# Kernel optimization log

Hardware: AMD Instinct MI355X
Metric: run time of the kernel (lower is better)

Reference implementation:

```python
import jax, jax.numpy as jnp
import numpy as np

N_PTS = 2048
NUM_GABOR = 2
IMG_H = 512
IMG_W = 512
CHUNK = 32  # gaussians per scan step
ALPHA_THRESH = 1.0 / 255.0


def setup_inputs() -> dict:
    key = jax.random.key(0)
    ks = jax.random.split(key, 6)
    xyz = jax.random.uniform(ks[0], (N_PTS, 2), dtype=jnp.float32) * jnp.array([IMG_W, IMG_H], jnp.float32)
    cov2d = jax.random.uniform(ks[1], (N_PTS, 3), dtype=jnp.float32)
    features_dc = jax.random.normal(ks[2], (N_PTS, 3), dtype=jnp.float32)
    opacity = jnp.ones((N_PTS, 1), jnp.float32)
    gabor_freqs = (jax.random.uniform(ks[3], (N_PTS * NUM_GABOR, 2), dtype=jnp.float32) - 0.5) * 0.002
    gabor_weights = jax.random.uniform(ks[4], (N_PTS * NUM_GABOR, 1), dtype=jnp.float32) * -5.0
    background = jnp.ones((3,), jnp.float32)
    return dict(xyz=xyz, cov2d=cov2d, features_dc=features_dc, opacity=opacity,
                gabor_freqs=gabor_freqs, gabor_weights=gabor_weights,
                background=background, H=IMG_H, W=IMG_W)


def _render(xyz, cov2d, features_dc, opacity, gabor_freqs, gabor_weights, H, W):
    n = xyz.shape[0]
    g = gabor_freqs.shape[0] // n
    dt = xyz.dtype
    # cov elements with lower bound (SLV=False branch)
    covs = cov2d + jnp.array([0.5, 0.0, 0.5], dt)
    sxx, sxy, syy = covs[:, 0], covs[:, 1], covs[:, 2]
    det = sxx * syy - sxy * sxy
    valid = det > 1e-8
    det_s = jnp.where(valid, det, 1.0)
    conic_a = syy / det_s
    conic_b = -sxy / det_s
    conic_c = sxx / det_s
    # radius from max eigenvalue (for visibility filter / radii output)
    mid = 0.5 * (sxx + syy)
    lam = mid + jnp.sqrt(jnp.maximum(mid * mid - det, 0.1))
    radii = jnp.where(valid, jnp.ceil(3.0 * jnp.sqrt(lam)), 0.0).astype(jnp.int32)

    colors = jax.nn.sigmoid(features_dc)                      # color_norm=True
    freqs = jnp.exp(gabor_freqs).reshape(n, g, 2)             # get_gabor_freqs
    gw = jax.nn.sigmoid(gabor_weights).reshape(n, g)          # get_gabor_weights

    px = (jnp.arange(W, dtype=dt) + 0.5)[None, :]             # (1, W)
    py = (jnp.arange(H, dtype=dt) + 0.5)[:, None]             # (H, 1)

    steps = n // CHUNK
    def chunked(a):
        return a.reshape((steps, CHUNK) + a.shape[1:])

    xs = (chunked(xyz[:, 0]), chunked(xyz[:, 1]),
          chunked(conic_a), chunked(conic_b), chunked(conic_c),
          chunked(opacity[:, 0]), chunked(colors),
          chunked(freqs[:, :, 0]), chunked(freqs[:, :, 1]),
          chunked(gw), chunked(valid))

    def body(acc, args):
        x, y, ca, cb, cc, op, col, fx, fy, w, vm = args
        dx = px[None, :, :] - x[:, None, None]                 # (C,1,W)
        dy = py[None, :, :] - y[:, None, None]                 # (C,H,1)
        sigma = 0.5 * (ca[:, None, None] * dx * dx + cc[:, None, None] * dy * dy) \
                + cb[:, None, None] * (dx * dy)                # (C,H,W)
        alpha = op[:, None, None] * jnp.exp(-sigma)
        alpha = jnp.minimum(alpha, 0.999)
        alpha = jnp.where((alpha < ALPHA_THRESH) | (~vm[:, None, None]), 0.0, alpha)
        # gabor modulation: 1 + sum_k w_k * cos(fx_k*dx + fy_k*dy)
        arg = fx[:, :, None, None] * dx[:, None, :, :] + fy[:, :, None, None] * dy[:, None, :, :]
        mod = 1.0 + jnp.sum(w[:, :, None, None] * jnp.cos(arg), axis=1)  # (C,H,W)
        wgt = alpha * mod
        acc = acc + jnp.einsum('nhw,nc->hwc', wgt, col)
        return acc, None

    out, _ = jax.lax.scan(body, jnp.zeros((H, W, 3), dt), xs)
    img = jnp.clip(out, 0.0, 1.0)                              # (H,W,3)
    render = jnp.transpose(img[None], (0, 3, 1, 2))            # (1,3,H,W)
    return render, radii


def reference(xyz, cov2d, features_dc, opacity, gabor_freqs, gabor_weights, background, H, W):
    render, radii = _render(xyz, cov2d, features_dc, opacity, gabor_freqs, gabor_weights, H, W)
    visibility = radii > 0
    return render, radii, visibility
```

## Files before the change

### kernel.cpp

```cpp
#include <hip/hip_runtime.h>
#include <math.h>

#define NPTS 2048
#define NG 2
#define IMG_H 512
#define IMG_W 512
#define HW (IMG_H * IMG_W)
#define RENDER_SIZE (3 * HW)
#define S_MAX 5.5412636f

__device__ __forceinline__ float sigmoidf_(float x) {
    return 1.0f / (1.0f + expf(-x));
}

__global__ void init_kernel(const float* __restrict__ cov2d, float* __restrict__ out) {
    int i = blockIdx.x * blockDim.x + threadIdx.x;
    if (i < RENDER_SIZE) out[i] = 0.0f;
    if (i < NPTS) {
        float sxx = cov2d[i * 3 + 0] + 0.5f;
        float sxy = cov2d[i * 3 + 1];
        float syy = cov2d[i * 3 + 2] + 0.5f;
        float det = __fsub_rn(__fmul_rn(sxx, syy), __fmul_rn(sxy, sxy));
        bool valid = det > 1e-8f;
        float mid = __fmul_rn(0.5f, __fadd_rn(sxx, syy));
        float t = __fsub_rn(__fmul_rn(mid, mid), det);
        t = fmaxf(t, 0.1f);
        float lam = __fadd_rn(mid, sqrtf(t));
        float r = valid ? ceilf(__fmul_rn(3.0f, sqrtf(lam))) : 0.0f;
        out[RENDER_SIZE + i] = r;
        out[RENDER_SIZE + NPTS + i] = (r > 0.0f) ? 1.0f : 0.0f;
    }
}

__global__ __launch_bounds__(64) void splat_kernel(
    const float* __restrict__ xyz, const float* __restrict__ cov2d,
    const float* __restrict__ fdc, const float* __restrict__ opac,
    const float* __restrict__ gfreq, const float* __restrict__ gwts,
    float* __restrict__ out)
{
    int p = blockIdx.x;
    float sxx = cov2d[p * 3 + 0] + 0.5f;
    float sxy = cov2d[p * 3 + 1];
    float syy = cov2d[p * 3 + 2] + 0.5f;
    float det = sxx * syy - sxy * sxy;
    if (!(det > 1e-8f)) return;

    float inv = 1.0f / det;
    float ca = syy * inv;
    float cb = -sxy * inv;
    float cc = sxx * inv;

    float xn = xyz[p * 2 + 0];
    float yn = xyz[p * 2 + 1];
    float op = opac[p];

    float c0 = sigmoidf_(fdc[p * 3 + 0]);
    float c1 = sigmoidf_(fdc[p * 3 + 1]);
    float c2 = sigmoidf_(fdc[p * 3 + 2]);

    float fx0 = expf(gfreq[(p * NG + 0) * 2 + 0]);
    float fy0 = expf(gfreq[(p * NG + 0) * 2 + 1]);
    float fx1 = expf(gfreq[(p * NG + 1) * 2 + 0]);
    float fy1 = expf(gfreq[(p * NG + 1) * 2 + 1]);
    float w0 = sigmoidf_(gwts[p * NG + 0]);
    float w1 = sigmoidf_(gwts[p * NG + 1]);

    float dxm = sqrtf(2.0f * S_MAX * sxx) + 0.01f;
    float dym = sqrtf(2.0f * S_MAX * syy) + 0.01f;
    int x0 = max(0, (int)ceilf(xn - dxm - 0.5f));
    int x1 = min(IMG_W - 1, (int)floorf(xn + dxm - 0.5f));
    int y0 = max(0, (int)ceilf(yn - dym - 0.5f));
    int y1 = min(IMG_H - 1, (int)floorf(yn + dym - 0.5f));
    int bw = x1 - x0 + 1;
    int bh = y1 - y0 + 1;
    if (bw <= 0 || bh <= 0) return;
    int area = bw * bh;

    for (int idx = threadIdx.x; idx < area; idx += 64) {
        int ix = x0 + idx % bw;
        int iy = y0 + idx / bw;
        float dx = (ix + 0.5f) - xn;
        float dy = (iy + 0.5f) - yn;
        float sigma = 0.5f * (ca * dx * dx + cc * dy * dy) + cb * (dx * dy);
        float alpha = op * expf(-sigma);
        alpha = fminf(alpha, 0.999f);
        if (alpha < (1.0f / 255.0f)) continue;
        float mod = 1.0f + w0 * cosf(fx0 * dx + fy0 * dy)
                         + w1 * cosf(fx1 * dx + fy1 * dy);
        float wgt = alpha * mod;
        int pix = iy * IMG_W + ix;
        atomicAdd(&out[pix],          wgt * c0);
        atomicAdd(&out[HW + pix],     wgt * c1);
        atomicAdd(&out[2 * HW + pix], wgt * c2);
    }
}

__global__ void clamp_kernel(float* __restrict__ out) {
    int i = blockIdx.x * blockDim.x + threadIdx.x;
    if (i < RENDER_SIZE) {
        float v = out[i];
        out[i] = fminf(fmaxf(v, 0.0f), 1.0f);
    }
}

extern "C" void kernel_launch(void* const* d_in, const int* in_sizes, int n_in,
                              void* d_out, int out_size, void* d_ws, size_t ws_size,
                              hipStream_t stream) {
    const float* xyz   = (const float*)d_in[0];
    const float* cov2d = (const float*)d_in[1];
    const float* fdc   = (const float*)d_in[2];
    const float* opac  = (const float*)d_in[3];
    const float* gfreq = (const float*)d_in[4];
    const float* gwts  = (const float*)d_in[5];
    float* out = (float*)d_out;

    int blocks = (RENDER_SIZE + 255) / 256;
    init_kernel<<<blocks, 256, 0, stream>>>(cov2d, out);
    splat_kernel<<<NPTS, 64, 0, stream>>>(xyz, cov2d, fdc, opac, gfreq, gwts, out);
    clamp_kernel<<<blocks, 256, 0, stream>>>(out);
}
```

Baseline: 79.25 us.

## Replace atomic point splatting with per-tile gather rendering in one fused kernel

Switches from per-gaussian blocks that atomically scatter into the image to per-tile blocks (32x8 pixels) that cull gaussians in chunks into shared memory and accumulate per-pixel in registers. Radii computation, zero-init and clamping are fused into the same kernel, removing two full-image passes and two launches. The trade-off is that every tile re-reads and culls all points, and each chunk adds barrier synchronisation.

After: 82.83 us. 1.05x slower.

```diff
diff --git a/kernel.cpp b/kernel.cpp
--- a/kernel.cpp
+++ b/kernel.cpp
@@ -8,99 +8,126 @@
 #define HW (IMG_H * IMG_W)
 #define RENDER_SIZE (3 * HW)
 #define S_MAX 5.5412636f
+#define ALPHA_THRESH (1.0f / 255.0f)
+
+#define TW 32
+#define TH 8
+#define TILES_X (IMG_W / TW)
+#define TILES_Y (IMG_H / TH)
+#define NTILES (TILES_X * TILES_Y)
+#define CHUNK_PTS 256
 
 __device__ __forceinline__ float sigmoidf_(float x) {
     return 1.0f / (1.0f + expf(-x));
 }
 
-__global__ void init_kernel(const float* __restrict__ cov2d, float* __restrict__ out) {
-    int i = blockIdx.x * blockDim.x + threadIdx.x;
-    if (i < RENDER_SIZE) out[i] = 0.0f;
-    if (i < NPTS) {
-        float sxx = cov2d[i * 3 + 0] + 0.5f;
-        float sxy = cov2d[i * 3 + 1];
-        float syy = cov2d[i * 3 + 2] + 0.5f;
-        float det = __fsub_rn(__fmul_rn(sxx, syy), __fmul_rn(sxy, sxy));
-        bool valid = det > 1e-8f;
-        float mid = __fmul_rn(0.5f, __fadd_rn(sxx, syy));
-        float t = __fsub_rn(__fmul_rn(mid, mid), det);
-        t = fmaxf(t, 0.1f);
-        float lam = __fadd_rn(mid, sqrtf(t));
-        float r = valid ? ceilf(__fmul_rn(3.0f, sqrtf(lam))) : 0.0f;
-        out[RENDER_SIZE + i] = r;
-        out[RENDER_SIZE + NPTS + i] = (r > 0.0f) ? 1.0f : 0.0f;
-    }
-}
-
-__global__ __launch_bounds__(64) void splat_kernel(
+__global__ __launch_bounds__(256) void render_kernel(
     const float* __restrict__ xyz, const float* __restrict__ cov2d,
     const float* __restrict__ fdc, const float* __restrict__ opac,
     const float* __restrict__ gfreq, const float* __restrict__ gwts,
     float* __restrict__ out)
 {
-    int p = blockIdx.x;
-    float sxx = cov2d[p * 3 + 0] + 0.5f;
-    float sxy = cov2d[p * 3 + 1];
-    float syy = cov2d[p * 3 + 2] + 0.5f;
-    float det = sxx * syy - sxy * sxy;
-    if (!(det > 1e-8f)) return;
+    __shared__ float s_xn[CHUNK_PTS], s_yn[CHUNK_PTS];
+    __shared__ float s_ca[CHUNK_PTS], s_cb[CHUNK_PTS], s_cc[CHUNK_PTS];
+    __shared__ float s_op[CHUNK_PTS];
+    __shared__ float s_c0[CHUNK_PTS], s_c1[CHUNK_PTS], s_c2[CHUNK_PTS];
+    __shared__ float s_fx0[CHUNK_PTS], s_fy0[CHUNK_PTS];
+    __shared__ float s_fx1[CHUNK_PTS], s_fy1[CHUNK_PTS];
+    __shared__ float s_w0[CHUNK_PTS], s_w1[CHUNK_PTS];
+    __shared__ int s_cnt;
 
-    float inv = 1.0f / det;
-    float ca = syy * inv;
-    float cb = -sxy * inv;
-    float cc = sxx * inv;
+    const int t = threadIdx.x;
+    const int tile = blockIdx.x;
+    const int tx0 = (tile % TILES_X) * TW;
+    const int ty0 = (tile / TILES_X) * TH;
+    const int ix = tx0 + (t % TW);
+    const int iy = ty0 + (t / TW);
+    const float pxf = ix + 0.5f;
+    const float pyf = iy + 0.5f;
 
-    float xn = xyz[p * 2 + 0];
-    float yn = xyz[p * 2 + 1];
-    float op = opac[p];
+    if (tile < NPTS / CHUNK_PTS) {
+        int p = tile * CHUNK_PTS + t;
+        float sxx = cov2d[p * 3 + 0] + 0.5f;
+        float sxy = cov2d[p * 3 + 1];
+        float syy = cov2d[p * 3 + 2] + 0.5f;
+        float det = __fsub_rn(__fmul_rn(sxx, syy), __fmul_rn(sxy, sxy));
+        bool valid = det > 1e-8f;
+        float mid = __fmul_rn(0.5f, __fadd_rn(sxx, syy));
+        float q = fmaxf(__fsub_rn(__fmul_rn(mid, mid), det), 0.1f);
+        float lam = __fadd_rn(mid, sqrtf(q));
+        float r = valid ? ceilf(__fmul_rn(3.0f, sqrtf(lam))) : 0.0f;
+        out[RENDER_SIZE + p] = r;
+        out[RENDER_SIZE + NPTS + p] = (r > 0.0f) ? 1.0f : 0.0f;
+    }
 
-    float c0 = sigmoidf_(fdc[p * 3 + 0]);
-    float c1 = sigmoidf_(fdc[p * 3 + 1]);
-    float c2 = sigmoidf_(fdc[p * 3 + 2]);
+    const float txlo = tx0 + 0.5f, txhi = tx0 + (TW - 1) + 0.5f;
+    const float tylo = ty0 + 0.5f, tyhi = ty0 + (TH - 1) + 0.5f;
 
-    float fx0 = expf(gfreq[(p * NG + 0) * 2 + 0]);
-    float fy0 = expf(gfreq[(p * NG + 0) * 2 + 1]);
-    float fx1 = expf(gfreq[(p * NG + 1) * 2 + 0]);
-    float fy1 = expf(gfreq[(p * NG + 1) * 2 + 1]);
-    float w0 = sigmoidf_(gwts[p * NG + 0]);
-    float w1 = sigmoidf_(gwts[p * NG + 1]);
+    float acc0 = 0.0f, acc1 = 0.0f, acc2 = 0.0f;
 
-    float dxm = sqrtf(2.0f * S_MAX * sxx) + 0.01f;
-    float dym = sqrtf(2.0f * S_MAX * syy) + 0.01f;
-    int x0 = max(0, (int)ceilf(xn - dxm - 0.5f));
-    int x1 = min(IMG_W - 1, (int)floorf(xn + dxm - 0.5f));
-    int y0 = max(0, (int)ceilf(yn - dym - 0.5f));
-    int y1 = min(IMG_H - 1, (int)floorf(yn + dym - 0.5f));
-    int bw = x1 - x0 + 1;
-    int bh = y1 - y0 + 1;
-    if (bw <= 0 || bh <= 0) return;
-    int area = bw * bh;
+    for (int c = 0; c < NPTS / CHUNK_PTS; ++c) {
+        const int p = c * CHUNK_PTS + t;
 
-    for (int idx = threadIdx.x; idx < area; idx += 64) {
-        int ix = x0 + idx % bw;
-        int iy = y0 + idx / bw;
-        float dx = (ix + 0.5f) - xn;
-        float dy = (iy + 0.5f) - yn;
-        float sigma = 0.5f * (ca * dx * dx + cc * dy * dy) + cb * (dx * dy);
-        float alpha = op * expf(-sigma);
-        alpha = fminf(alpha, 0.999f);
-        if (alpha < (1.0f / 255.0f)) continue;
-        float mod = 1.0f + w0 * cosf(fx0 * dx + fy0 * dy)
-                         + w1 * cosf(fx1 * dx + fy1 * dy);
-        float wgt = alpha * mod;
-        int pix = iy * IMG_W + ix;
-        atomicAdd(&out[pix],          wgt * c0);
-        atomicAdd(&out[HW + pix],     wgt * c1);
-        atomicAdd(&out[2 * HW + pix], wgt * c2);
+        float sxx = cov2d[p * 3 + 0] + 0.5f;
+        float sxy = cov2d[p * 3 + 1];
+        float syy = cov2d[p * 3 + 2] + 0.5f;
+        float det = sxx * syy - sxy * sxy;
+        float xn = xyz[p * 2 + 0];
+        float yn = xyz[p * 2 + 1];
+        float dxm = sqrtf(2.0f * S_MAX * sxx) + 0.01f;
+        float dym = sqrtf(2.0f * S_MAX * syy) + 0.01f;
+        bool ok = (det > 1e-8f)
+               && (xn - dxm <= txhi) && (xn + dxm >= txlo)
+               && (yn - dym <= tyhi) && (yn + dym >= tylo);
+
+        __syncthreads();
+        if (t == 0) s_cnt = 0;
+        __syncthreads();
+
+        if (ok) {
+            int slot = atomicAdd(&s_cnt, 1);
+            float inv = 1.0f / det;
+            s_ca[slot] = syy * inv;
+            s_cb[slot] = -sxy * inv;
+            s_cc[slot] = sxx * inv;
+            s_xn[slot] = xn;
+            s_yn[slot] = yn;
+            s_op[slot] = opac[p];
+            s_c0[slot] = sigmoidf_(fdc[p * 3 + 0]);
+            s_c1[slot] = sigmoidf_(fdc[p * 3 + 1]);
+            s_c2[slot] = sigmoidf_(fdc[p * 3 + 2]);
+            s_fx0[slot] = expf(gfreq[p * 4 + 0]);
+            s_fy0[slot] = expf(gfreq[p * 4 + 1]);
+            s_fx1[slot] = expf(gfreq[p * 4 + 2]);
+            s_fy1[slot] = expf(gfreq[p * 4 + 3]);
+            s_w0[slot] = sigmoidf_(gwts[p * 2 + 0]);
+            s_w1[slot] = sigmoidf_(gwts[p * 2 + 1]);
+        }
+        __syncthreads();
+
+        const int n = s_cnt;
+        for (int s = 0; s < n; ++s) {
+            float dx = pxf - s_xn[s];
+            float dy = pyf - s_yn[s];
+            float sigma = 0.5f * (s_ca[s] * dx * dx + s_cc[s] * dy * dy)
+                        + s_cb[s] * (dx * dy);
+            float alpha = fminf(s_op[s] * expf(-sigma), 0.999f);
+            if (alpha >= ALPHA_THRESH) {
+                float mod = 1.0f
+                    + s_w0[s] * cosf(s_fx0[s] * dx + s_fy0[s] * dy)
+                    + s_w1[s] * cosf(s_fx1[s] * dx + s_fy1[s] * dy);
+                float wgt = alpha * mod;
+                acc0 = fmaf(wgt, s_c0[s], acc0);
+                acc1 = fmaf(wgt, s_c1[s], acc1);
+                acc2 = fmaf(wgt, s_c2[s], acc2);
+            }
+        }
     }
-}
 
-__global__ void clamp_kernel(float* __restrict__ out) {
-    int i = blockIdx.x * blockDim.x + threadIdx.x;
-    if (i < RENDER_SIZE) {
-        float v = out[i];
-        out[i] = fminf(fmaxf(v, 0.0f), 1.0f);
-    }
+    const int pix = iy * IMG_W + ix;
+    out[pix]          = fminf(fmaxf(acc0, 0.0f), 1.0f);
+    out[HW + pix]     = fminf(fmaxf(acc1, 0.0f), 1.0f);
+    out[2 * HW + pix] = fminf(fmaxf(acc2, 0.0f), 1.0f);
 }
 
 extern "C" void kernel_launch(void* const* d_in, const int* in_sizes, int n_in,
@@ -114,8 +141,5 @@
     const float* gwts  = (const float*)d_in[5];
     float* out = (float*)d_out;
 
-    int blocks = (RENDER_SIZE + 255) / 256;
-    init_kernel<<<blocks, 256, 0, stream>>>(cov2d, out);
-    splat_kernel<<<NPTS, 64, 0, stream>>>(xyz, cov2d, fdc, opac, gfreq, gwts, out);
-    clamp_kernel<<<blocks, 256, 0, stream>>>(out);
+    render_kernel<<<NTILES, 256, 0, stream>>>(xyz, cov2d, fdc, opac, gfreq, gwts, out);
 }
```
